# Optimization experiments

Measured on AMD Instinct MI355X. Metric: run time of the kernel, lower is better.

## Reference

```python
import jax, jax.numpy as jnp
import numpy as np
import math

EPS = 1e-5

def setnorm(x, w, b):
    # normalize over (samples, features) per batch element, then per-feature scale/shift
    m = jnp.mean(x, axis=(1, 2), keepdims=True)
    s = jnp.sqrt(jnp.mean(jnp.square(x - m), axis=(1, 2), keepdims=True) + EPS)
    return (x - m) / s * w + b

def setup_inputs() -> dict:
    key = jax.random.key(0)
    ks = jax.random.split(key, 8)
    B, Nx, Ny, dX, dY = 4, 2048, 2048, 256, 256
    sX, sY = 1.0 / math.sqrt(dX), 1.0 / math.sqrt(dY)
    return {
        'X': jax.random.normal(ks[0], (B, Nx, dX), jnp.float32),
        'Y': jax.random.normal(ks[1], (B, Ny, dY), jnp.float32),
        'Wq': jax.random.normal(ks[2], (dY, dX), jnp.float32) * sX,
        'bq': jnp.zeros((dY,), jnp.float32),
        'Wk': jax.random.normal(ks[3], (dY, dY), jnp.float32) * sY,
        'bk': jnp.zeros((dY,), jnp.float32),
        'Wv': jax.random.normal(ks[4], (dY, dY), jnp.float32) * sY,
        'bv': jnp.zeros((dY,), jnp.float32),
        'Wo': jax.random.normal(ks[5], (dX, dY), jnp.float32) * sY,
        'bo': jnp.zeros((dX,), jnp.float32),
        'Wres': jax.random.normal(ks[6], (dX, dX), jnp.float32) * sX,
        'bres': jnp.zeros((dX,), jnp.float32),
        'nq_w': jnp.ones((dX,), jnp.float32), 'nq_b': jnp.zeros((dX,), jnp.float32),
        'nk_w': jnp.ones((dY,), jnp.float32), 'nk_b': jnp.zeros((dY,), jnp.float32),
        'n0_w': jnp.ones((dX,), jnp.float32), 'n0_b': jnp.zeros((dX,), jnp.float32),
    }

def reference(X, Y, Wq, bq, Wk, bk, Wv, bv, Wo, bo, Wres, bres,
              nq_w, nq_b, nk_w, nk_b, n0_w, n0_b):
    num_heads = 8
    dim_Y = Wq.shape[0]
    d = dim_Y // num_heads
    B, Nx, _ = X.shape
    Ny = Y.shape[1]

    Q = setnorm(X, nq_w, nq_b) @ Wq.T + bq          # [B, Nx, dY]
    K = setnorm(Y, nk_w, nk_b) @ Wk.T + bk          # [B, Ny, dY]
    V = Y @ Wv.T + bv                               # [B, Ny, dY]

    # split into heads along feature dim (matches torch split/cat over dim 0)
    Qh = Q.reshape(B, Nx, num_heads, d)
    Kh = K.reshape(B, Ny, num_heads, d)
    Vh = V.reshape(B, Ny, num_heads, d)

    # NOTE: original scales by sqrt(dim_Y), not sqrt(head_dim)
    scores = jnp.einsum('bqhd,bkhd->bhqk', Qh, Kh) / math.sqrt(dim_Y)
    A = jax.nn.softmax(scores, axis=-1)             # [B, H, Nx, Ny]
    Oh = jnp.einsum('bhqk,bkhd->bqhd', A, Vh)       # [B, Nx, H, d]
    O = Oh.reshape(B, Nx, dim_Y) @ Wo.T + bo        # [B, Nx, dX]

    H = X + O
    H = H + jax.nn.relu(setnorm(H, n0_w, n0_b)) @ Wres.T + bres
    return H
```

## Files before the change

### kernel.cpp

```cpp
#include <hip/hip_runtime.h>


typedef _Float16 f16;
typedef _Float16 f16x4 __attribute__((ext_vector_type(4)));
typedef _Float16 f16x8 __attribute__((ext_vector_type(8)));
typedef float f32x4 __attribute__((ext_vector_type(4)));
typedef unsigned int u32;
typedef unsigned int u32x2 __attribute__((ext_vector_type(2)));

#define DEV static __device__ __forceinline__

DEV void load_lds16(const void* g, void* s) {
  __builtin_amdgcn_global_load_lds(
      (const __attribute__((address_space(1))) void*)g,
      (__attribute__((address_space(3))) void*)s, 16, 0, 0);
}

DEV float fexp2(float x) {
  float r;
  asm("v_exp_f32 %0, %1" : "=v"(r) : "v"(x));
  return r;
}

DEV u32 pkh(float a, float b) {
  auto h = __builtin_amdgcn_cvt_pkrtz(a, b);
  return __builtin_bit_cast(u32, h);
}

__global__ __launch_bounds__(256) void stats_partial(const float* __restrict__ p0,
                                                     const float* __restrict__ p1,
                                                     float2* __restrict__ partial) {
  const int s = blockIdx.y;
  const float* p = (s >= 4 ? p1 + (size_t)(s - 4) * 524288 : p0 + (size_t)s * 524288)
                   + (size_t)blockIdx.x * 8192;
  float sum = 0.f, ss = 0.f;
#pragma unroll
  for (int j = 0; j < 8; ++j) {
    f32x4 v = *reinterpret_cast<const f32x4*>(p + (size_t)(j * 256 + threadIdx.x) * 4);
#pragma unroll
    for (int e = 0; e < 4; ++e) { sum += v[e]; ss += v[e] * v[e]; }
  }
#pragma unroll
  for (int m = 1; m < 64; m <<= 1) { sum += __shfl_xor(sum, m); ss += __shfl_xor(ss, m); }
  __shared__ float2 red[4];
  if ((threadIdx.x & 63) == 0) red[threadIdx.x >> 6] = make_float2(sum, ss);
  __syncthreads();
  if (threadIdx.x == 0) {
    float a = 0.f, b = 0.f;
    for (int i = 0; i < 4; ++i) { a += red[i].x; b += red[i].y; }
    partial[s * 64 + blockIdx.x] = make_float2(a, b);
  }
}

DEV float2 finalize_stats(const float2* __restrict__ partial, int s) {
  const int lane = threadIdx.x & 63;
  float2 v = partial[s * 64 + lane];
  float sum = v.x, ss = v.y;
#pragma unroll
  for (int m = 1; m < 64; m <<= 1) { sum += __shfl_xor(sum, m); ss += __shfl_xor(ss, m); }
  const float invN = 1.f / 524288.f;
  const float mean = sum * invN;
  const float var = fmaxf(ss * invN - mean * mean, 0.f);
  return make_float2(mean, rsqrtf(var + 1e-5f));
}

__global__ __launch_bounds__(256) void prep_xy(const float* __restrict__ X,
                                               const float* __restrict__ Y,
                                               f16* __restrict__ Xn, f16* __restrict__ Yn,
                                               f16* __restrict__ Yc,
                                               const float2* __restrict__ partial,
                                               const float* __restrict__ nqw, const float* __restrict__ nqb,
                                               const float* __restrict__ nkw, const float* __restrict__ nkb) {
  const int bid = blockIdx.x;
  const bool isX = bid < 1024;
  const size_t idx = ((size_t)(isX ? bid : bid - 1024) * 256 + threadIdx.x) * 8;
  const int slice = (int)(idx >> 19);
  const float2 st = finalize_stats(partial, (isX ? 0 : 4) + slice);
  const int f = (int)(idx & 255);
  const float* in = isX ? X : Y;
  f32x4 v0 = *reinterpret_cast<const f32x4*>(in + idx);
  f32x4 v1 = *reinterpret_cast<const f32x4*>(in + idx + 4);
  const float* wv = isX ? nqw : nkw;
  const float* bv = isX ? nqb : nkb;
  f32x4 w0 = *reinterpret_cast<const f32x4*>(wv + f);
  f32x4 w1 = *reinterpret_cast<const f32x4*>(wv + f + 4);
  f32x4 b0 = *reinterpret_cast<const f32x4*>(bv + f);
  f32x4 b1 = *reinterpret_cast<const f32x4*>(bv + f + 4);
  f16x8 on;
#pragma unroll
  for (int j = 0; j < 4; ++j) {
    on[j]     = (f16)((v0[j] - st.x) * st.y * w0[j] + b0[j]);
    on[j + 4] = (f16)((v1[j] - st.x) * st.y * w1[j] + b1[j]);
  }
  if (isX) {
    *reinterpret_cast<f16x8*>(Xn + idx) = on;
  } else {
    *reinterpret_cast<f16x8*>(Yn + idx) = on;
    f16x8 oc;
#pragma unroll
    for (int j = 0; j < 4; ++j) { oc[j] = (f16)v0[j]; oc[j + 4] = (f16)v1[j]; }
    *reinterpret_cast<f16x8*>(Yc + idx) = oc;
  }
}

__global__ __launch_bounds__(256) void prep_h(const float* __restrict__ H, f16* __restrict__ out,
                                              const float2* __restrict__ partial,
                                              const float* __restrict__ w, const float* __restrict__ b) {
  const size_t idx = ((size_t)blockIdx.x * 256 + threadIdx.x) * 8;
  const float2 st = finalize_stats(partial, (int)(idx >> 19));
  const int f = (int)(idx & 255);
  f32x4 v0 = *reinterpret_cast<const f32x4*>(H + idx);
  f32x4 v1 = *reinterpret_cast<const f32x4*>(H + idx + 4);
  f32x4 w0 = *reinterpret_cast<const f32x4*>(w + f);
  f32x4 w1 = *reinterpret_cast<const f32x4*>(w + f + 4);
  f32x4 b0 = *reinterpret_cast<const f32x4*>(b + f);
  f32x4 b1 = *reinterpret_cast<const f32x4*>(b + f + 4);
  f16x8 o;
#pragma unroll
  for (int j = 0; j < 4; ++j) {
    o[j]     = (f16)fmaxf((v0[j] - st.x) * st.y * w0[j] + b0[j], 0.f);
    o[j + 4] = (f16)fmaxf((v1[j] - st.x) * st.y * w1[j] + b1[j], 0.f);
  }
  *reinterpret_cast<f16x8*>(out + idx) = o;
}

__global__ __launch_bounds__(256) void cast_w(const float* __restrict__ w0, const float* __restrict__ w1,
                                              const float* __restrict__ w2, const float* __restrict__ w3,
                                              const float* __restrict__ w4, f16* __restrict__ out) {
  const int i8 = blockIdx.x * 256 + threadIdx.x;
  const int mat = i8 >> 13;
  const size_t off = (size_t)(i8 & 8191) * 8;
  const float* src = mat == 0 ? w0 : mat == 1 ? w1 : mat == 2 ? w2 : mat == 3 ? w3 : w4;
  f32x4 v0 = *reinterpret_cast<const f32x4*>(src + off);
  f32x4 v1 = *reinterpret_cast<const f32x4*>(src + off + 4);
  f16x8 o;
#pragma unroll
  for (int j = 0; j < 4; ++j) { o[j] = (f16)v0[j]; o[j + 4] = (f16)v1[j]; }
  *reinterpret_cast<f16x8*>(out + (size_t)mat * 65536 + off) = o;
}

enum { GM_F16 = 0, GM_VT = 1, GM_F32R = 2 };

struct GemmPtrs {
  const f16* A; const f16* W; const float* bias; const float* resid;
  void* out; float scale; int mode;
};

template <bool QKV>
__global__ __launch_bounds__(256) void gemm_nt(const f16* __restrict__ A0, const f16* __restrict__ A1,
                                               const f16* __restrict__ A2, const f16* __restrict__ Wc,
                                               const float* __restrict__ b0, const float* __restrict__ b1,
                                               const float* __restrict__ b2,
                                               const float* __restrict__ resid,
                                               void* o0p, void* o1p, void* o2p,
                                               float scale0, int mode0) {
  __shared__ __align__(16) f16 lds[2][8192];
  const int t = threadIdx.x;
  const int w = t >> 6, lane = t & 63;
  const int g = lane >> 4, lq = lane & 15;
  const int m0 = blockIdx.x * 64, n0 = blockIdx.y * 64;
  const int wr = (w >> 1) * 32, wc = (w & 1) * 32;
  const int z = QKV ? blockIdx.z : 0;

  const f16* A = QKV ? (z == 0 ? A0 : z == 1 ? A1 : A2) : A0;
  const f16* W = QKV ? (Wc + z * 65536) : Wc;
  const float* bias = QKV ? (z == 0 ? b0 : z == 1 ? b1 : b2) : b0;
  void* outp = QKV ? (z == 0 ? o0p : z == 1 ? o1p : o2p) : o0p;
  const float scale = (QKV && z != 0) ? 1.f : scale0;
  const int mode = QKV ? (z == 2 ? GM_VT : GM_F16) : mode0;

  const int r_ = t >> 2, c0 = t & 3, sw = (t >> 3) & 3;
  const int kgA = (c0 ^ sw) << 3;
  const f16* gA = A + (size_t)(m0 + r_) * 256 + kgA;
  const f16* gB = W + (size_t)(n0 + r_) * 256 + kgA;
  f16* dA0 = &lds[0][0] + t * 8;
  f16* dA1 = &lds[1][0] + t * 8;

  f32x4 acc[2][2] = {};

  auto stage = [&](int kt, int buf) {
    f16* base = buf ? dA1 : dA0;
    const int ko = kt * 64;
    load_lds16(gA + ko, base);
    load_lds16(gA + ko + 32, base + 2048);
    load_lds16(gB + ko, base + 4096);
    load_lds16(gB + ko + 32, base + 6144);
  };

  const int swr = ((lq >> 1) & 3);
  auto compute = [&](int buf) {
    const f16* L = &lds[buf][0];
#pragma unroll
    for (int kk = 0; kk < 2; ++kk) {
      f16x8 af[2], bf[2];
#pragma unroll
      for (int i = 0; i < 2; ++i)
        af[i] = *reinterpret_cast<const f16x8*>(L + kk * 2048 + (wr + i * 16 + lq) * 32 + ((g ^ swr) << 3));
#pragma unroll
      for (int j = 0; j < 2; ++j)
        bf[j] = *reinterpret_cast<const f16x8*>(L + 4096 + kk * 2048 + (wc + j * 16 + lq) * 32 + ((g ^ swr) << 3));
#pragma unroll
      for (int i = 0; i < 2; ++i)
#pragma unroll
        for (int j = 0; j < 2; ++j)
          acc[i][j] = __builtin_amdgcn_mfma_f32_16x16x32_f16(af[i], bf[j], acc[i][j], 0, 0, 0);
    }
  };

  stage(0, 0);
  __syncthreads();
  stage(1, 1); compute(0); __syncthreads();
  stage(2, 0); compute(1); __syncthreads();
  stage(3, 1); compute(0); __syncthreads();
  compute(1);

#pragma unroll
  for (int i = 0; i < 2; ++i)
#pragma unroll
    for (int j = 0; j < 2; ++j) {
      const int row0 = m0 + wr + i * 16 + g * 4;
      const int col = n0 + wc + j * 16 + lq;
      const float bv = bias[col];
#pragma unroll
      for (int r = 0; r < 4; ++r) {
        const int rr = row0 + r;
        float v = (acc[i][j][r] + bv) * scale;
        if (mode == GM_F16) {
          ((f16*)outp)[(size_t)rr * 256 + col] = (f16)v;
        } else if (mode == GM_VT) {
          ((f16*)outp)[((size_t)(rr >> 11) * 256 + col) * 2048 + (rr & 2047)] = (f16)v;
        } else {
          const size_t o = (size_t)rr * 256 + col;
          ((float*)outp)[o] = v + resid[o];
        }
      }
    }
}

__global__ __launch_bounds__(256) void attn_kernel(const f16* __restrict__ Q,
                                                   const f16* __restrict__ K,
                                                   const f16* __restrict__ Vt,
                                                   f16* __restrict__ O) {
  __shared__ __align__(16) f16 kbuf[2][2048];
  __shared__ __align__(16) f16 vbuf[2][2048];
  __shared__ __align__(16) f16 plds[4][1024];
  const int t = threadIdx.x;
  const int w = t >> 6, lane = t & 63;
  const int g = lane >> 4, lq = lane & 15;
  const int wg = blockIdx.x;
  const int linear = (wg & 7) * 128 + (wg >> 3);
  const int qt = linear & 31;
  const int hb = linear >> 5;
  const int h = hb & 7, b = hb >> 3;
  const int q0 = qt * 64 + w * 16;
  const float THR = 8.0f;

  const f16* Kb = K + (size_t)b * 2048 * 256 + h * 32;
  const f16* Vb = Vt + ((size_t)b * 256 + h * 32) * 2048;
  f16* myp = plds[w];

  const f16x8 qf =
      *reinterpret_cast<const f16x8*>(Q + (size_t)(b * 2048 + q0 + lq) * 256 + h * 32 + g * 8);

  const f16* gK = Kb + (size_t)(t >> 2) * 256 +
                  (((t & 3) ^ ((t >> 2) & 3) ^ ((t >> 4) & 3)) << 3);
  const f16* gV = Vb + (size_t)(t >> 3) * 2048 + ((((t & 7) ^ ((t >> 3) & 7))) << 3);
  f16* dKa = &kbuf[0][0] + t * 8;
  f16* dKb = &kbuf[1][0] + t * 8;
  f16* dVa = &vbuf[0][0] + t * 8;
  f16* dVb = &vbuf[1][0] + t * 8;
  const int KSTEP = 64 * 256;

  const int swk = ((g ^ (lq & 3) ^ ((lq >> 2) & 3)) << 3);
  const int kro = lq * 32 + swk;
  const int svA = ((g ^ (lq & 7)) << 3);
  const int svB = (((4 + g) ^ (lq & 7)) << 3);
  const int vr0 = lq * 64, vr1 = (16 + lq) * 64;

  const int xq = (lq & 7) << 3;
  f16* wp0 = myp + ((lq * 64 + g * 4 + 0) ^ xq);
  f16* wp1 = myp + ((lq * 64 + g * 4 + 16) ^ xq);
  f16* wp2 = myp + ((lq * 64 + g * 4 + 32) ^ xq);
  f16* wp3 = myp + ((lq * 64 + g * 4 + 48) ^ xq);
  const f16* rp0 = myp + ((lq * 64 + 0 + g * 8) ^ xq);
  const f16* rp1 = myp + ((lq * 64 + 32 + g * 8) ^ xq);

  f32x4 o0 = {0.f, 0.f, 0.f, 0.f}, o1 = {0.f, 0.f, 0.f, 0.f};
  float m_ = -1e30f;
  float l_ = 0.f;

  auto compute = [&](int buf) {
    const f16* kb = &kbuf[buf][0];
    const f16* vb = &vbuf[buf][0];
    f16x8 kf0 = *reinterpret_cast<const f16x8*>(kb + kro);
    f16x8 kf1 = *reinterpret_cast<const f16x8*>(kb + 512 + kro);
    f16x8 kf2 = *reinterpret_cast<const f16x8*>(kb + 1024 + kro);
    f16x8 kf3 = *reinterpret_cast<const f16x8*>(kb + 1536 + kro);

    const f32x4 z = {0.f, 0.f, 0.f, 0.f};
    __builtin_amdgcn_s_setprio(1);
    f32x4 s0 = __builtin_amdgcn_mfma_f32_16x16x32_f16(kf0, qf, z, 0, 0, 0);
    f32x4 s1 = __builtin_amdgcn_mfma_f32_16x16x32_f16(kf1, qf, z, 0, 0, 0);
    f32x4 s2 = __builtin_amdgcn_mfma_f32_16x16x32_f16(kf2, qf, z, 0, 0, 0);
    f32x4 s3 = __builtin_amdgcn_mfma_f32_16x16x32_f16(kf3, qf, z, 0, 0, 0);
    __builtin_amdgcn_s_setprio(0);

    float t0 = fmaxf(fmaxf(s0[0], s0[1]), s0[2]);
    float t1 = fmaxf(fmaxf(s0[3], s1[0]), s1[1]);
    float t2 = fmaxf(fmaxf(s1[2], s1[3]), s2[0]);
    float t3 = fmaxf(fmaxf(s2[1], s2[2]), s2[3]);
    float t4 = fmaxf(fmaxf(s3[0], s3[1]), s3[2]);
    float x = fmaxf(fmaxf(fmaxf(t0, t1), fmaxf(t2, t3)), fmaxf(t4, s3[3]));
    x = fmaxf(x, __shfl_xor(x, 16));
    x = fmaxf(x, __shfl_xor(x, 32));

    if (__any(x > m_ + THR)) {
      const float mnew = fmaxf(m_, x);
      const float sc = fexp2(m_ - mnew);
      m_ = mnew;
      l_ *= sc;
#pragma unroll
      for (int r = 0; r < 4; ++r) {
        const float scq = __shfl(sc, g * 4 + r);
        o0[r] *= scq;
        o1[r] *= scq;
      }
    }

    float e00 = fexp2(s0[0] - m_), e01 = fexp2(s0[1] - m_), e02 = fexp2(s0[2] - m_), e03 = fexp2(s0[3] - m_);
    float e10 = fexp2(s1[0] - m_), e11 = fexp2(s1[1] - m_), e12 = fexp2(s1[2] - m_), e13 = fexp2(s1[3] - m_);
    float e20 = fexp2(s2[0] - m_), e21 = fexp2(s2[1] - m_), e22 = fexp2(s2[2] - m_), e23 = fexp2(s2[3] - m_);
    float e30 = fexp2(s3[0] - m_), e31 = fexp2(s3[1] - m_), e32 = fexp2(s3[2] - m_), e33 = fexp2(s3[3] - m_);
    const float la = (e00 + e01) + (e02 + e03);
    const float lb = (e10 + e11) + (e12 + e13);
    const float lc = (e20 + e21) + (e22 + e23);
    const float ld = (e30 + e31) + (e32 + e33);
    l_ += (la + lb) + (lc + ld);

    u32x2 w0q = {pkh(e00, e01), pkh(e02, e03)};
    u32x2 w1q = {pkh(e10, e11), pkh(e12, e13)};
    u32x2 w2q = {pkh(e20, e21), pkh(e22, e23)};
    u32x2 w3q = {pkh(e30, e31), pkh(e32, e33)};
    *reinterpret_cast<u32x2*>(wp0) = w0q;
    *reinterpret_cast<u32x2*>(wp1) = w1q;
    *reinterpret_cast<u32x2*>(wp2) = w2q;
    *reinterpret_cast<u32x2*>(wp3) = w3q;

    f16x8 pa0 = *reinterpret_cast<const f16x8*>(rp0);
    f16x8 pa1 = *reinterpret_cast<const f16x8*>(rp1);
    f16x8 v00 = *reinterpret_cast<const f16x8*>(vb + vr0 + svA);
    f16x8 v01 = *reinterpret_cast<const f16x8*>(vb + vr0 + svB);
    f16x8 v10 = *reinterpret_cast<const f16x8*>(vb + vr1 + svA);
    f16x8 v11 = *reinterpret_cast<const f16x8*>(vb + vr1 + svB);
    __builtin_amdgcn_s_setprio(1);
    o0 = __builtin_amdgcn_mfma_f32_16x16x32_f16(pa0, v00, o0, 0, 0, 0);
    o1 = __builtin_amdgcn_mfma_f32_16x16x32_f16(pa0, v10, o1, 0, 0, 0);
    o0 = __builtin_amdgcn_mfma_f32_16x16x32_f16(pa1, v01, o0, 0, 0, 0);
    o1 = __builtin_amdgcn_mfma_f32_16x16x32_f16(pa1, v11, o1, 0, 0, 0);
    __builtin_amdgcn_s_setprio(0);
  };

  load_lds16(gK, dKa);
  load_lds16(gV, dVa);
  gK += KSTEP; gV += 64;
  __syncthreads();

  for (int kt = 0; kt < 32; kt += 2) {
    load_lds16(gK, dKb);
    load_lds16(gV, dVb);
    gK += KSTEP; gV += 64;
    compute(0);
    __syncthreads();
    if (kt < 30) {
      load_lds16(gK, dKa);
      load_lds16(gV, dVa);
      gK += KSTEP; gV += 64;
    }
    compute(1);
    __syncthreads();
  }

  float lf = l_ + __shfl_xor(l_, 16);
  lf += __shfl_xor(lf, 32);
#pragma unroll
  for (int r = 0; r < 4; ++r) {
    const float lr = __shfl(lf, g * 4 + r);
    const float inv = 1.f / lr;
    const size_t row = (size_t)b * 2048 + q0 + g * 4 + r;
    O[row * 256 + h * 32 + lq] = (f16)(o0[r] * inv);
    O[row * 256 + h * 32 + 16 + lq] = (f16)(o1[r] * inv);
  }
}

extern "C" void kernel_launch(void* const* d_in, const int* in_sizes, int n_in,
                              void* d_out, int out_size, void* d_ws, size_t ws_size,
                              hipStream_t stream) {
  (void)in_sizes; (void)n_in; (void)out_size; (void)ws_size;
  const float* X    = (const float*)d_in[0];
  const float* Y    = (const float*)d_in[1];
  const float* Wq   = (const float*)d_in[2];
  const float* bq   = (const float*)d_in[3];
  const float* Wk   = (const float*)d_in[4];
  const float* bk   = (const float*)d_in[5];
  const float* Wv   = (const float*)d_in[6];
  const float* bv   = (const float*)d_in[7];
  const float* Wo   = (const float*)d_in[8];
  const float* bo   = (const float*)d_in[9];
  const float* Wres = (const float*)d_in[10];
  const float* bres = (const float*)d_in[11];
  const float* nq_w = (const float*)d_in[12];
  const float* nq_b = (const float*)d_in[13];
  const float* nk_w = (const float*)d_in[14];
  const float* nk_b = (const float*)d_in[15];
  const float* n0_w = (const float*)d_in[16];
  const float* n0_b = (const float*)d_in[17];
  float* out = (float*)d_out;

  char* ws = (char*)d_ws;
  const size_t MB = 1u << 20;
  f16* bufXn = (f16*)(ws + 0 * MB);
  f16* bufYn = (f16*)(ws + 4 * MB);
  f16* bufYc = (f16*)(ws + 8 * MB);
  f16* bufQ  = (f16*)(ws + 12 * MB);
  f16* bufK  = (f16*)(ws + 16 * MB);
  f16* bufVt = (f16*)(ws + 20 * MB);
  f16* bufW  = (f16*)(ws + 24 * MB);
  float2* partial = (float2*)(ws + 24 * MB + 700 * 1024);

  stats_partial<<<dim3(64, 8), 256, 0, stream>>>(X, Y, partial);

  cast_w<<<160, 256, 0, stream>>>(Wq, Wk, Wv, Wo, Wres, bufW);
  prep_xy<<<2048, 256, 0, stream>>>(X, Y, bufXn, bufYn, bufYc, partial,
                                    nq_w, nq_b, nk_w, nk_b);

  const float qscale = 1.4426950408889634f / 16.f;
  gemm_nt<true><<<dim3(128, 4, 3), 256, 0, stream>>>(
      bufXn, bufYn, bufYc, bufW, bq, bk, bv, nullptr,
      bufQ, bufK, bufVt, qscale, GM_F16);

  attn_kernel<<<1024, 256, 0, stream>>>(bufQ, bufK, bufVt, bufXn);

  gemm_nt<false><<<dim3(128, 4), 256, 0, stream>>>(
      bufXn, nullptr, nullptr, bufW + 3 * 65536, bo, nullptr, nullptr, X,
      out, nullptr, nullptr, 1.f, GM_F32R);

  stats_partial<<<dim3(64, 4), 256, 0, stream>>>(out, out, partial);
  prep_h<<<1024, 256, 0, stream>>>(out, bufYc, partial, n0_w, n0_b);

  gemm_nt<false><<<dim3(128, 4), 256, 0, stream>>>(
      bufYc, nullptr, nullptr, bufW + 4 * 65536, bres, nullptr, nullptr, out,
      out, nullptr, nullptr, 1.f, GM_F32R);
}
```

Baseline: 104.3 us.

## Process two query tiles per wave in attention to reuse K/V loads

Each attention workgroup now handles 128 query rows instead of 64, with each wave computing two independent 16-row query blocks against the same K/V tiles staged in LDS. The grid is halved to 512 blocks and the P scratch buffer doubled. This halves global K/V traffic and LDS K/V fragment reads per query and gives more independent MFMA work to interleave with softmax. The cost is more registers per wave, larger LDS, and fewer workgroups (512 across the CUs), which may lower occupancy and latency hiding.

```diff
diff --git a/kernel.cpp b/kernel.cpp
--- a/kernel.cpp
+++ b/kernel.cpp
@@ -141,11 +141,6 @@
 
 enum { GM_F16 = 0, GM_VT = 1, GM_F32R = 2 };
 
-struct GemmPtrs {
-  const f16* A; const f16* W; const float* bias; const float* resid;
-  void* out; float scale; int mode;
-};
-
 template <bool QKV>
 __global__ __launch_bounds__(256) void gemm_nt(const f16* __restrict__ A0, const f16* __restrict__ A1,
                                                const f16* __restrict__ A2, const f16* __restrict__ Wc,
@@ -243,24 +238,27 @@
                                                    f16* __restrict__ O) {
   __shared__ __align__(16) f16 kbuf[2][2048];
   __shared__ __align__(16) f16 vbuf[2][2048];
-  __shared__ __align__(16) f16 plds[4][1024];
+  __shared__ __align__(16) f16 plds[4][2048];
   const int t = threadIdx.x;
   const int w = t >> 6, lane = t & 63;
   const int g = lane >> 4, lq = lane & 15;
   const int wg = blockIdx.x;
-  const int linear = (wg & 7) * 128 + (wg >> 3);
-  const int qt = linear & 31;
-  const int hb = linear >> 5;
+  const int linear = (wg & 7) * 64 + (wg >> 3);
+  const int qt = linear & 15;
+  const int hb = linear >> 4;
   const int h = hb & 7, b = hb >> 3;
-  const int q0 = qt * 64 + w * 16;
+  const int qA = qt * 128 + w * 16;
+  const int qB = qA + 64;
   const float THR = 8.0f;
 
   const f16* Kb = K + (size_t)b * 2048 * 256 + h * 32;
   const f16* Vb = Vt + ((size_t)b * 256 + h * 32) * 2048;
   f16* myp = plds[w];
 
-  const f16x8 qf =
-      *reinterpret_cast<const f16x8*>(Q + (size_t)(b * 2048 + q0 + lq) * 256 + h * 32 + g * 8);
+  const f16x8 qfA =
+      *reinterpret_cast<const f16x8*>(Q + (size_t)(b * 2048 + qA + lq) * 256 + h * 32 + g * 8);
+  const f16x8 qfB =
+      *reinterpret_cast<const f16x8*>(Q + (size_t)(b * 2048 + qB + lq) * 256 + h * 32 + g * 8);
 
   const f16* gK = Kb + (size_t)(t >> 2) * 256 +
                   (((t & 3) ^ ((t >> 2) & 3) ^ ((t >> 4) & 3)) << 3);
@@ -278,33 +276,20 @@
   const int vr0 = lq * 64, vr1 = (16 + lq) * 64;
 
   const int xq = (lq & 7) << 3;
-  f16* wp0 = myp + ((lq * 64 + g * 4 + 0) ^ xq);
-  f16* wp1 = myp + ((lq * 64 + g * 4 + 16) ^ xq);
-  f16* wp2 = myp + ((lq * 64 + g * 4 + 32) ^ xq);
-  f16* wp3 = myp + ((lq * 64 + g * 4 + 48) ^ xq);
-  const f16* rp0 = myp + ((lq * 64 + 0 + g * 8) ^ xq);
-  const f16* rp1 = myp + ((lq * 64 + 32 + g * 8) ^ xq);
-
-  f32x4 o0 = {0.f, 0.f, 0.f, 0.f}, o1 = {0.f, 0.f, 0.f, 0.f};
-  float m_ = -1e30f;
-  float l_ = 0.f;
-
-  auto compute = [&](int buf) {
-    const f16* kb = &kbuf[buf][0];
-    const f16* vb = &vbuf[buf][0];
-    f16x8 kf0 = *reinterpret_cast<const f16x8*>(kb + kro);
-    f16x8 kf1 = *reinterpret_cast<const f16x8*>(kb + 512 + kro);
-    f16x8 kf2 = *reinterpret_cast<const f16x8*>(kb + 1024 + kro);
-    f16x8 kf3 = *reinterpret_cast<const f16x8*>(kb + 1536 + kro);
-
-    const f32x4 z = {0.f, 0.f, 0.f, 0.f};
-    __builtin_amdgcn_s_setprio(1);
-    f32x4 s0 = __builtin_amdgcn_mfma_f32_16x16x32_f16(kf0, qf, z, 0, 0, 0);
-    f32x4 s1 = __builtin_amdgcn_mfma_f32_16x16x32_f16(kf1, qf, z, 0, 0, 0);
-    f32x4 s2 = __builtin_amdgcn_mfma_f32_16x16x32_f16(kf2, qf, z, 0, 0, 0);
-    f32x4 s3 = __builtin_amdgcn_mfma_f32_16x16x32_f16(kf3, qf, z, 0, 0, 0);
-    __builtin_amdgcn_s_setprio(0);
-
+  const int wb0 = (lq * 64 + g * 4 + 0) ^ xq;
+  const int wb1 = (lq * 64 + g * 4 + 16) ^ xq;
+  const int wb2 = (lq * 64 + g * 4 + 32) ^ xq;
+  const int wb3 = (lq * 64 + g * 4 + 48) ^ xq;
+  const int rb0 = (lq * 64 + 0 + g * 8) ^ xq;
+  const int rb1 = (lq * 64 + 32 + g * 8) ^ xq;
+
+  f32x4 o0A = {0.f, 0.f, 0.f, 0.f}, o1A = {0.f, 0.f, 0.f, 0.f};
+  f32x4 o0B = {0.f, 0.f, 0.f, 0.f}, o1B = {0.f, 0.f, 0.f, 0.f};
+  float mA = -1e30f, lA = 0.f;
+  float mB = -1e30f, lB = 0.f;
+
+  auto softmax = [&](f32x4 s0, f32x4 s1, f32x4 s2, f32x4 s3,
+                     float& m_, float& l_, f32x4& o0, f32x4& o1, f16* pbase) {
     float t0 = fmaxf(fmaxf(s0[0], s0[1]), s0[2]);
     float t1 = fmaxf(fmaxf(s0[3], s1[0]), s1[1]);
     float t2 = fmaxf(fmaxf(s1[2], s1[3]), s2[0]);
@@ -313,7 +298,6 @@
     float x = fmaxf(fmaxf(fmaxf(t0, t1), fmaxf(t2, t3)), fmaxf(t4, s3[3]));
     x = fmaxf(x, __shfl_xor(x, 16));
     x = fmaxf(x, __shfl_xor(x, 32));
-
     if (__any(x > m_ + THR)) {
       const float mnew = fmaxf(m_, x);
       const float sc = fexp2(m_ - mnew);
@@ -326,7 +310,6 @@
         o1[r] *= scq;
       }
     }
-
     float e00 = fexp2(s0[0] - m_), e01 = fexp2(s0[1] - m_), e02 = fexp2(s0[2] - m_), e03 = fexp2(s0[3] - m_);
     float e10 = fexp2(s1[0] - m_), e11 = fexp2(s1[1] - m_), e12 = fexp2(s1[2] - m_), e13 = fexp2(s1[3] - m_);
     float e20 = fexp2(s2[0] - m_), e21 = fexp2(s2[1] - m_), e22 = fexp2(s2[2] - m_), e23 = fexp2(s2[3] - m_);
@@ -336,27 +319,58 @@
     const float lc = (e20 + e21) + (e22 + e23);
     const float ld = (e30 + e31) + (e32 + e33);
     l_ += (la + lb) + (lc + ld);
-
     u32x2 w0q = {pkh(e00, e01), pkh(e02, e03)};
     u32x2 w1q = {pkh(e10, e11), pkh(e12, e13)};
     u32x2 w2q = {pkh(e20, e21), pkh(e22, e23)};
     u32x2 w3q = {pkh(e30, e31), pkh(e32, e33)};
-    *reinterpret_cast<u32x2*>(wp0) = w0q;
-    *reinterpret_cast<u32x2*>(wp1) = w1q;
-    *reinterpret_cast<u32x2*>(wp2) = w2q;
-    *reinterpret_cast<u32x2*>(wp3) = w3q;
-
-    f16x8 pa0 = *reinterpret_cast<const f16x8*>(rp0);
-    f16x8 pa1 = *reinterpret_cast<const f16x8*>(rp1);
+    *reinterpret_cast<u32x2*>(pbase + wb0) = w0q;
+    *reinterpret_cast<u32x2*>(pbase + wb1) = w1q;
+    *reinterpret_cast<u32x2*>(pbase + wb2) = w2q;
+    *reinterpret_cast<u32x2*>(pbase + wb3) = w3q;
+  };
+
+  auto compute = [&](int buf) {
+    const f16* kb = &kbuf[buf][0];
+    const f16* vb = &vbuf[buf][0];
+    f16x8 kf0 = *reinterpret_cast<const f16x8*>(kb + kro);
+    f16x8 kf1 = *reinterpret_cast<const f16x8*>(kb + 512 + kro);
+    f16x8 kf2 = *reinterpret_cast<const f16x8*>(kb + 1024 + kro);
+    f16x8 kf3 = *reinterpret_cast<const f16x8*>(kb + 1536 + kro);
+    const f32x4 z = {0.f, 0.f, 0.f, 0.f};
+
+    __builtin_amdgcn_s_setprio(1);
+    f32x4 a0 = __builtin_amdgcn_mfma_f32_16x16x32_f16(kf0, qfA, z, 0, 0, 0);
+    f32x4 a1 = __builtin_amdgcn_mfma_f32_16x16x32_f16(kf1, qfA, z, 0, 0, 0);
+    f32x4 a2 = __builtin_amdgcn_mfma_f32_16x16x32_f16(kf2, qfA, z, 0, 0, 0);
+    f32x4 a3 = __builtin_amdgcn_mfma_f32_16x16x32_f16(kf3, qfA, z, 0, 0, 0);
+    __builtin_amdgcn_s_setprio(0);
+    softmax(a0, a1, a2, a3, mA, lA, o0A, o1A, myp);
+
+    __builtin_amdgcn_s_setprio(1);
+    f32x4 c0 = __builtin_amdgcn_mfma_f32_16x16x32_f16(kf0, qfB, z, 0, 0, 0);
+    f32x4 c1 = __builtin_amdgcn_mfma_f32_16x16x32_f16(kf1, qfB, z, 0, 0, 0);
+    f32x4 c2 = __builtin_amdgcn_mfma_f32_16x16x32_f16(kf2, qfB, z, 0, 0, 0);
+    f32x4 c3 = __builtin_amdgcn_mfma_f32_16x16x32_f16(kf3, qfB, z, 0, 0, 0);
+    __builtin_amdgcn_s_setprio(0);
+    softmax(c0, c1, c2, c3, mB, lB, o0B, o1B, myp + 1024);
+
     f16x8 v00 = *reinterpret_cast<const f16x8*>(vb + vr0 + svA);
     f16x8 v01 = *reinterpret_cast<const f16x8*>(vb + vr0 + svB);
     f16x8 v10 = *reinterpret_cast<const f16x8*>(vb + vr1 + svA);
     f16x8 v11 = *reinterpret_cast<const f16x8*>(vb + vr1 + svB);
+    f16x8 paA0 = *reinterpret_cast<const f16x8*>(myp + rb0);
+    f16x8 paA1 = *reinterpret_cast<const f16x8*>(myp + rb1);
+    f16x8 paB0 = *reinterpret_cast<const f16x8*>(myp + 1024 + rb0);
+    f16x8 paB1 = *reinterpret_cast<const f16x8*>(myp + 1024 + rb1);
     __builtin_amdgcn_s_setprio(1);
-    o0 = __builtin_amdgcn_mfma_f32_16x16x32_f16(pa0, v00, o0, 0, 0, 0);
-    o1 = __builtin_amdgcn_mfma_f32_16x16x32_f16(pa0, v10, o1, 0, 0, 0);
-    o0 = __builtin_amdgcn_mfma_f32_16x16x32_f16(pa1, v01, o0, 0, 0, 0);
-    o1 = __builtin_amdgcn_mfma_f32_16x16x32_f16(pa1, v11, o1, 0, 0, 0);
+    o0A = __builtin_amdgcn_mfma_f32_16x16x32_f16(paA0, v00, o0A, 0, 0, 0);
+    o1A = __builtin_amdgcn_mfma_f32_16x16x32_f16(paA0, v10, o1A, 0, 0, 0);
+    o0A = __builtin_amdgcn_mfma_f32_16x16x32_f16(paA1, v01, o0A, 0, 0, 0);
+    o1A = __builtin_amdgcn_mfma_f32_16x16x32_f16(paA1, v11, o1A, 0, 0, 0);
+    o0B = __builtin_amdgcn_mfma_f32_16x16x32_f16(paB0, v00, o0B, 0, 0, 0);
+    o1B = __builtin_amdgcn_mfma_f32_16x16x32_f16(paB0, v10, o1B, 0, 0, 0);
+    o0B = __builtin_amdgcn_mfma_f32_16x16x32_f16(paB1, v01, o0B, 0, 0, 0);
+    o1B = __builtin_amdgcn_mfma_f32_16x16x32_f16(paB1, v11, o1B, 0, 0, 0);
     __builtin_amdgcn_s_setprio(0);
   };
 
@@ -380,16 +394,20 @@
     __syncthreads();
   }
 
-  float lf = l_ + __shfl_xor(l_, 16);
-  lf += __shfl_xor(lf, 32);
-#pragma unroll
-  for (int r = 0; r < 4; ++r) {
-    const float lr = __shfl(lf, g * 4 + r);
-    const float inv = 1.f / lr;
-    const size_t row = (size_t)b * 2048 + q0 + g * 4 + r;
-    O[row * 256 + h * 32 + lq] = (f16)(o0[r] * inv);
-    O[row * 256 + h * 32 + 16 + lq] = (f16)(o1[r] * inv);
-  }
+  auto epilogue = [&](float l_, const f32x4& o0, const f32x4& o1, int q0) {
+    float lf = l_ + __shfl_xor(l_, 16);
+    lf += __shfl_xor(lf, 32);
+#pragma unroll
+    for (int r = 0; r < 4; ++r) {
+      const float lr = __shfl(lf, g * 4 + r);
+      const float inv = 1.f / lr;
+      const size_t row = (size_t)b * 2048 + q0 + g * 4 + r;
+      O[row * 256 + h * 32 + lq] = (f16)(o0[r] * inv);
+      O[row * 256 + h * 32 + 16 + lq] = (f16)(o1[r] * inv);
+    }
+  };
+  epilogue(lA, o0A, o1A, qA);
+  epilogue(lB, o0B, o1B, qB);
 }
 
 extern "C" void kernel_launch(void* const* d_in, const int* in_sizes, int n_in,
@@ -438,7 +456,7 @@
       bufXn, bufYn, bufYc, bufW, bq, bk, bv, nullptr,
       bufQ, bufK, bufVt, qscale, GM_F16);
 
-  attn_kernel<<<1024, 256, 0, stream>>>(bufQ, bufK, bufVt, bufXn);
+  attn_kernel<<<512, 256, 0, stream>>>(bufQ, bufK, bufVt, bufXn);
 
   gemm_nt<false><<<dim3(128, 4), 256, 0, stream>>>(
       bufXn, nullptr, nullptr, bufW + 3 * 65536, bo, nullptr, nullptr, X,
```

Measured after the change: 107.6 us. +3.2%, slower.
